# Kernel tuning notes

Hardware: AMD Instinct MI355X
Metric: run time of the kernel (lower is better)

The kernel has to match this reference:

```python
import jax, jax.numpy as jnp
import numpy as np

B, SQ, SE, H, NH = 2, 2048, 2048, 1024, 16
HD = H // NH  # 64

def setup_inputs() -> dict:
    key = jax.random.key(0)
    ks = jax.random.split(key, 8)
    s = 1.0 / np.sqrt(H)
    return {
        "hidden_states": jax.random.normal(ks[0], (B, SQ, H), jnp.float32),
        "encoder_hidden_states": jax.random.normal(ks[1], (B, SE, H), jnp.float32),
        "attention_mask": jnp.zeros((B, 1, 1, SQ + SE), jnp.float32),
        "Wq": jax.random.normal(ks[2], (H, H), jnp.float32) * s,
        "bq": jnp.zeros((H,), jnp.float32),
        "Wk": jax.random.normal(ks[3], (H, H), jnp.float32) * s,
        "bk": jnp.zeros((H,), jnp.float32),
        "Wv": jax.random.normal(ks[4], (H, H), jnp.float32) * s,
        "bv": jnp.zeros((H,), jnp.float32),
    }

def _split_heads(x):
    # [B, S, H] -> [B, NH, S, HD]
    b, s, _ = x.shape
    return x.reshape(b, s, NH, HD).transpose(0, 2, 1, 3)

def reference(hidden_states, encoder_hidden_states, attention_mask, Wq, bq, Wk, bk, Wv, bv):
    # Q from self tokens; K,V from concat(self, encoder) along sequence
    all_hs = jnp.concatenate([hidden_states, encoder_hidden_states], axis=1)  # [B, SQ+SE, H]
    q = _split_heads(hidden_states @ Wq + bq)   # [B, NH, SQ, HD]
    k = _split_heads(all_hs @ Wk + bk)          # [B, NH, SKV, HD]
    v = _split_heads(all_hs @ Wv + bv)          # [B, NH, SKV, HD]
    scores = jnp.einsum('bhqd,bhkd->bhqk', q, k) / jnp.sqrt(jnp.float32(HD))
    scores = scores + attention_mask            # additive mask, broadcast [B,1,1,SKV]
    probs = jax.nn.softmax(scores, axis=-1)     # dropout p=0 (eval)
    ctx = jnp.einsum('bhqk,bhkd->bhqd', probs, v)
    ctx = ctx.transpose(0, 2, 1, 3).reshape(hidden_states.shape[0], hidden_states.shape[1], H)
    return ctx
```

## Files before the change

### kernel.cpp

```cpp
#include <hip/hip_runtime.h>
#include <hip/hip_bf16.h>
#include <stdint.h>


typedef __attribute__((ext_vector_type(8))) short short8;
typedef __attribute__((ext_vector_type(4))) float f32x4;
typedef __attribute__((ext_vector_type(4))) unsigned short us4;

typedef __attribute__((ext_vector_type(8), may_alias)) short short8a;
typedef __attribute__((may_alias)) unsigned long long u64a;

#define MEMBAR() asm volatile("" ::: "memory")
#define DEV static __device__ __forceinline__

DEV unsigned short f2bf(float f) {
  unsigned int u = __builtin_bit_cast(unsigned int, f);
  u += 0x7fffu + ((u >> 16) & 1u);
  return (unsigned short)(u >> 16);
}

DEV float exp2_(float x) {
#if __has_builtin(__builtin_amdgcn_exp2f)
  return __builtin_amdgcn_exp2f(x);
#else
  float r; asm("v_exp_f32 %0, %1" : "=v"(r) : "v"(x)); return r;
#endif
}

DEV unsigned int cvtpk_bf16(float lo, float hi) {
  unsigned int r;
  asm("v_cvt_pk_bf16_f32 %0, %1, %2" : "=v"(r) : "v"(lo), "v"(hi));
  return r;
}

DEV void g2lds16(const void* g, void* l) {
  __builtin_amdgcn_global_load_lds((const __attribute__((address_space(1))) void*)g,
                                   (__attribute__((address_space(3))) void*)l, 16, 0, 0);
}

__global__ __launch_bounds__(256) void convert_allhs(const float* __restrict__ hid,
                                                     const float* __restrict__ enc,
                                                     unsigned short* __restrict__ ah) {
  int idx = blockIdx.x * 256 + threadIdx.x;
  const int perB = 4096 * 256;
  int b = idx / perB, r = idx - b * perB;
  int s = r >> 8, c4 = r & 255;
  const float* srcrow = (s < 2048) ? hid + (size_t)(b * 2048 + s) * 1024
                                   : enc + (size_t)(b * 2048 + (s - 2048)) * 1024;
  f32x4 v = *(const f32x4*)(srcrow + c4 * 4);
  us4 o;
  o[0] = f2bf(v[0]); o[1] = f2bf(v[1]); o[2] = f2bf(v[2]); o[3] = f2bf(v[3]);
  *(us4*)(ah + (size_t)idx * 4) = o;
}

__global__ __launch_bounds__(256) void premul_mask(const float* __restrict__ m,
                                                   float* __restrict__ o) {
  int i = blockIdx.x * 256 + threadIdx.x;
  o[i] = m[i] * 1.4426950408889634f;
}

__global__ __launch_bounds__(256) void transpose_w3(const float* __restrict__ Wq,
                                                    const float* __restrict__ Wk,
                                                    const float* __restrict__ Wv,
                                                    unsigned short* __restrict__ WtBase) {
  __shared__ unsigned short t[64][65];
  const int z = blockIdx.z;
  const float* W = (z == 0) ? Wq : (z == 1) ? Wk : Wv;
  unsigned short* Wt = WtBase + (size_t)z * 1048576;
  int k0 = blockIdx.y * 64, n0 = blockIdx.x * 64;
  int tid = threadIdx.x;
#pragma unroll
  for (int rep = 0; rep < 16; rep++) {
    int idx = rep * 256 + tid;
    int kk = idx >> 6, nn = idx & 63;
    t[kk][nn] = f2bf(W[(size_t)(k0 + kk) * 1024 + n0 + nn]);
  }
  __syncthreads();
#pragma unroll
  for (int rep = 0; rep < 16; rep++) {
    int idx = rep * 256 + tid;
    int nn = idx >> 6, kk = idx & 63;
    Wt[(size_t)(n0 + nn) * 1024 + k0 + kk] = t[kk][nn];
  }
}

__global__ __launch_bounds__(256) void gemm_all(const unsigned short* __restrict__ WTQ,
                                                const unsigned short* __restrict__ WTK,
                                                const unsigned short* __restrict__ WTV,
                                                const unsigned short* __restrict__ AH,
                                                const float* __restrict__ bq,
                                                const float* __restrict__ bk,
                                                const float* __restrict__ bv,
                                                unsigned short* __restrict__ Qout,
                                                unsigned short* __restrict__ Kout,
                                                unsigned short* __restrict__ Vout,
                                                float qscale) {
  __shared__ unsigned short ldsA[128 * 32];
  __shared__ unsigned short ldsB[128 * 32];

  int id = blockIdx.x;
  int f2 = (id & 7) * 160 + (id >> 3);

  const unsigned short *A, *Bm;
  const float* bias;
  unsigned short* outb;
  int S, mode, r0, c0;
  float osc = 1.0f;
  if (f2 < 256) {
    int t = f2;
    int b = t >> 7; t &= 127;
    c0 = (t & 15) * 128; r0 = (t >> 4) * 128;
    A = WTQ; Bm = AH + (size_t)b * 4194304; bias = bq;
    outb = Qout + (size_t)b * 2097152; S = 2048; mode = 0; osc = qscale;
  } else if (f2 < 768) {
    int t = f2 - 256;
    int b = t >> 8; t &= 255;
    c0 = (t & 31) * 128; r0 = (t >> 5) * 128;
    A = WTK; Bm = AH + (size_t)b * 4194304; bias = bk;
    outb = Kout + (size_t)b * 4194304; S = 4096; mode = 0;
  } else {
    int t = f2 - 768;
    int b = t >> 8; t &= 255;
    c0 = (t & 7) * 128; r0 = (t >> 3) * 128;
    A = AH + (size_t)b * 4194304; Bm = WTV; bias = bv;
    outb = Vout + (size_t)b * 4194304; S = 4096; mode = 1;
  }

  const int tid = threadIdx.x, w = tid >> 6, l = tid & 63;
  const int wr = w >> 1, wc = w & 1;
  const int lrow = l >> 2, lk = (l & 3) * 8;
  const int lc = l & 15, g = l >> 4;

  f32x4 acc[4][4];
#pragma unroll
  for (int i = 0; i < 4; i++)
#pragma unroll
    for (int j = 0; j < 4; j++) acc[i][j] = (f32x4){0.f, 0.f, 0.f, 0.f};

  for (int k0 = 0; k0 < 1024; k0 += 32) {
#pragma unroll
    for (int t = 0; t < 2; t++) {
      const int tt = w * 2 + t;
      g2lds16(A + (size_t)(r0 + tt * 16 + lrow) * 1024 + k0 + lk, (char*)ldsA + tt * 1024);
      g2lds16(Bm + (size_t)(c0 + tt * 16 + lrow) * 1024 + k0 + lk, (char*)ldsB + tt * 1024);
    }
    __syncthreads();
    short8 af[4], bf[4];
#pragma unroll
    for (int f = 0; f < 4; f++) {
      af[f] = *(const short8*)((const char*)ldsA + (wr * 64 + f * 16 + lc) * 64 + g * 16);
      bf[f] = *(const short8*)((const char*)ldsB + (wc * 64 + f * 16 + lc) * 64 + g * 16);
    }
#pragma unroll
    for (int fr = 0; fr < 4; fr++)
#pragma unroll
      for (int fc = 0; fc < 4; fc++)
        acc[fr][fc] = __builtin_amdgcn_mfma_f32_16x16x32_bf16(af[fr], bf[fc], acc[fr][fc], 0, 0, 0);
    __syncthreads();
  }

#pragma unroll
  for (int fr = 0; fr < 4; fr++) {
    int rb = r0 + wr * 64 + fr * 16 + g * 4;
    float bv4[4];
    if (mode == 0) {
#pragma unroll
      for (int i = 0; i < 4; i++) bv4[i] = bias[rb + i];
    }
#pragma unroll
    for (int fc = 0; fc < 4; fc++) {
      int c = c0 + wc * 64 + fc * 16 + lc;
      float bc = (mode == 0) ? 0.f : bias[c];
      us4 pk;
#pragma unroll
      for (int i = 0; i < 4; i++) {
        float v = (acc[fr][fc][i] + (mode == 0 ? bv4[i] : bc)) * osc;
        pk[i] = f2bf(v);
      }
      size_t addr;
      if (mode == 0) addr = ((size_t)(rb >> 6) * S + c) * 64 + (rb & 63);
      else           addr = (size_t)c * S + rb;
      *(us4*)(outb + addr) = pk;
    }
  }
}

__global__ __launch_bounds__(256) void attn_kernel(const unsigned short* __restrict__ Q,
                                                   const unsigned short* __restrict__ K,
                                                   const unsigned short* __restrict__ Vt,
                                                   const float* __restrict__ mask2,
                                                   float* __restrict__ out) {
  __shared__ __align__(16) char ldsKV[16384];
  __shared__ unsigned short plds[4096];
  char* ldsK = ldsKV;
  char* ldsV = ldsKV + 8192;

  int flat = blockIdx.x + 32 * (blockIdx.y + 16 * blockIdx.z);
  int xc = flat & 7, tt = flat >> 3;
  int f2 = xc * 64 + (tt & 63) + (tt >> 6) * 512;
  const int qt = f2 & 31, h = (f2 >> 5) & 15, b = f2 >> 9;

  const int tid = threadIdx.x, w = tid >> 6, l = tid & 63;
  const int lc = l & 15, g = l >> 4;

  const unsigned short* Qb = Q + ((size_t)(b * 16 + h) * 2048) * 64;
  const unsigned short* Kb = K + ((size_t)(b * 16 + h) * 4096) * 64;
  const unsigned short* Vb = Vt + ((size_t)(b * 16 + h) * 64) * 4096;
  const float* mk = mask2 + (size_t)b * 4096;
  const int sq0 = qt * 64 + w * 16;

  const int srow = l >> 3;
  const int schunk = (l & 7) ^ srow;

  short8 qf[2];
#pragma unroll
  for (int hh = 0; hh < 2; hh++)
    qf[hh] = *(const short8*)(Qb + (size_t)(sq0 + lc) * 64 + hh * 32 + g * 8);

  short8 ones;
#pragma unroll
  for (int i = 0; i < 8; i++) ones[i] = (short)0x3f80;

  f32x4 ctx[4];
#pragma unroll
  for (int df = 0; df < 4; df++) ctx[df] = (f32x4){0.f, 0.f, 0.f, 0.f};
  f32x4 lsacc = (f32x4){0.f, 0.f, 0.f, 0.f};

  char* pwave = (char*)plds + w * 2048;
  const int swz = (lc & 7) << 4;

  {
    short8 kreg[2], vreg[2];
#pragma unroll
    for (int c = 0; c < 2; c++) {
      int call = w * 2 + c;
      int r = call * 8 + srow;
      kreg[c] = *(const short8*)(Kb + (size_t)r * 64 + schunk * 8);
      vreg[c] = *(const short8*)(Vb + (size_t)r * 4096 + schunk * 8);
    }
#pragma unroll
    for (int c = 0; c < 2; c++) {
      int call = w * 2 + c;
      *(short8a*)(ldsK + call * 1024 + l * 16) = kreg[c];
      *(short8a*)(ldsV + call * 1024 + l * 16) = vreg[c];
    }
  }
  __syncthreads();

  for (int t = 0; t < 64; t++) {
    const int s0 = t * 64;

    f32x4 mvv[4];
#pragma unroll
    for (int f = 0; f < 4; f++)
      mvv[f] = *(const f32x4*)(mk + s0 + f * 16 + g * 4);

    short8 kreg[2], vreg[2];
    if (t < 63) {
#pragma unroll
      for (int c = 0; c < 2; c++) {
        int call = w * 2 + c;
        int r = call * 8 + srow;
        kreg[c] = *(const short8*)(Kb + (size_t)(s0 + 64 + r) * 64 + schunk * 8);
        vreg[c] = *(const short8*)(Vb + (size_t)r * 4096 + (s0 + 64) + schunk * 8);
      }
    }

#pragma unroll
    for (int f = 0; f < 4; f++) {
      short8 k0 = *(const short8*)(ldsK + (f * 16 + lc) * 128 + ((g ^ (lc & 7)) << 4));
      short8 k1 = *(const short8*)(ldsK + (f * 16 + lc) * 128 + (((4 + g) ^ (lc & 7)) << 4));
      f32x4 z = __builtin_amdgcn_mfma_f32_16x16x32_bf16(k0, qf[0], mvv[f], 0, 0, 0);
      z = __builtin_amdgcn_mfma_f32_16x16x32_bf16(k1, qf[1], z, 0, 0, 0);
      unsigned int lo = cvtpk_bf16(exp2_(z[0]), exp2_(z[1]));
      unsigned int hi = cvtpk_bf16(exp2_(z[2]), exp2_(z[3]));
      int base = lc * 128 + f * 32 + g * 8;
      *(u64a*)(pwave + (base ^ swz)) = ((unsigned long long)hi << 32) | lo;
    }

    MEMBAR();

    short8 pfrag[2];
#pragma unroll
    for (int kk = 0; kk < 2; kk++)
      pfrag[kk] = (short8)*(const short8a*)(pwave + ((lc * 128 + kk * 64 + g * 16) ^ swz));
#pragma unroll
    for (int df = 0; df < 4; df++) {
      short8 v0 = *(const short8*)(ldsV + (df * 16 + lc) * 128 + ((g ^ (lc & 7)) << 4));
      short8 v1 = *(const short8*)(ldsV + (df * 16 + lc) * 128 + (((4 + g) ^ (lc & 7)) << 4));
      ctx[df] = __builtin_amdgcn_mfma_f32_16x16x32_bf16(v0, pfrag[0], ctx[df], 0, 0, 0);
      ctx[df] = __builtin_amdgcn_mfma_f32_16x16x32_bf16(v1, pfrag[1], ctx[df], 0, 0, 0);
    }
    lsacc = __builtin_amdgcn_mfma_f32_16x16x32_bf16(ones, pfrag[0], lsacc, 0, 0, 0);
    lsacc = __builtin_amdgcn_mfma_f32_16x16x32_bf16(ones, pfrag[1], lsacc, 0, 0, 0);

    __syncthreads();

    if (t < 63) {
#pragma unroll
      for (int c = 0; c < 2; c++) {
        int call = w * 2 + c;
        *(short8a*)(ldsK + call * 1024 + l * 16) = kreg[c];
        *(short8a*)(ldsV + call * 1024 + l * 16) = vreg[c];
      }
      __syncthreads();
    }
  }

  float inv = 1.f / lsacc[0];
  size_t row = (size_t)(b * 2048 + sq0 + lc);
#pragma unroll
  for (int df = 0; df < 4; df++) {
    f32x4 o = ctx[df] * inv;
    *(f32x4*)(out + row * 1024 + h * 64 + df * 16 + g * 4) = o;
  }
}

extern "C" void kernel_launch(void* const* d_in, const int* in_sizes, int n_in,
                              void* d_out, int out_size, void* d_ws, size_t ws_size,
                              hipStream_t stream) {
  const float* hid = (const float*)d_in[0];
  const float* enc = (const float*)d_in[1];
  const float* mask = (const float*)d_in[2];
  const float* Wq = (const float*)d_in[3];
  const float* bq = (const float*)d_in[4];
  const float* Wk = (const float*)d_in[5];
  const float* bk = (const float*)d_in[6];
  const float* Wv = (const float*)d_in[7];
  const float* bv = (const float*)d_in[8];

  unsigned short* ws = (unsigned short*)d_ws;
  unsigned short* WTQ = ws;
  unsigned short* WTK = ws + 1048576;
  unsigned short* WTV = ws + 2097152;
  unsigned short* AH  = ws + 3145728;
  unsigned short* Qb  = ws + 11534336;
  unsigned short* Kb  = ws + 15728640;
  unsigned short* VT  = ws + 24117248;
  float* mask2 = (float*)(ws + 32505856);

  const float QSCALE = 0.18033688011112042f;

  convert_allhs<<<8192, 256, 0, stream>>>(hid, enc, AH);
  premul_mask<<<32, 256, 0, stream>>>(mask, mask2);
  transpose_w3<<<dim3(16, 16, 3), 256, 0, stream>>>(Wq, Wk, Wv, WTQ);

  gemm_all<<<1280, 256, 0, stream>>>(WTQ, WTK, WTV, AH, bq, bk, bv, Qb, Kb, VT, QSCALE);

  attn_kernel<<<dim3(32, 16, 2), 256, 0, stream>>>(Qb, Kb, VT, mask2, (float*)d_out);
}
```

Baseline: 196.7 us.

## Split KV sequence across wave pairs and give each wave two query tiles

The attention kernel now assigns each wave 32 query rows (two 16-row tiles) instead of 16, and splits the 4096-long KV range into two halves handled by different wave pairs. Each pair has its own K/V LDS buffers and runs 32 iterations instead of 64. Partial context and row sums are combined through LDS at the end. Because the exponent has no running max, the two halves add directly. The aim is to reuse each K/V fragment load across two query tiles and halve the serial loop length, at the cost of more registers, more LDS, and a final reduction step.

Result: slower. 201.2 us (+2.3%).

```diff
diff --git a/kernel.cpp b/kernel.cpp
--- a/kernel.cpp
+++ b/kernel.cpp
@@ -8,7 +8,9 @@
 typedef __attribute__((ext_vector_type(4))) unsigned short us4;
 
 typedef __attribute__((ext_vector_type(8), may_alias)) short short8a;
+typedef __attribute__((ext_vector_type(4), may_alias)) float f32x4a;
 typedef __attribute__((may_alias)) unsigned long long u64a;
+typedef __attribute__((may_alias)) float floata;
 
 #define MEMBAR() asm volatile("" ::: "memory")
 #define DEV static __device__ __forceinline__
@@ -190,10 +192,9 @@
                                                    const unsigned short* __restrict__ Vt,
                                                    const float* __restrict__ mask2,
                                                    float* __restrict__ out) {
-  __shared__ __align__(16) char ldsKV[16384];
-  __shared__ unsigned short plds[4096];
-  char* ldsK = ldsKV;
-  char* ldsV = ldsKV + 8192;
+  __shared__ __align__(16) char ldsK[2][8192];
+  __shared__ __align__(16) char ldsV[2][8192];
+  __shared__ __align__(16) char plds[16384];
 
   int flat = blockIdx.x + 32 * (blockIdx.y + 16 * blockIdx.z);
   int xc = flat & 7, tt = flat >> 3;
@@ -201,53 +202,60 @@
   const int qt = f2 & 31, h = (f2 >> 5) & 15, b = f2 >> 9;
 
   const int tid = threadIdx.x, w = tid >> 6, l = tid & 63;
+  const int rg = w & 1, kh = w >> 1;
   const int lc = l & 15, g = l >> 4;
 
   const unsigned short* Qb = Q + ((size_t)(b * 16 + h) * 2048) * 64;
-  const unsigned short* Kb = K + ((size_t)(b * 16 + h) * 4096) * 64;
-  const unsigned short* Vb = Vt + ((size_t)(b * 16 + h) * 64) * 4096;
-  const float* mk = mask2 + (size_t)b * 4096;
-  const int sq0 = qt * 64 + w * 16;
+  const unsigned short* Kb = K + ((size_t)((b * 16 + h) * 4096 + kh * 2048)) * 64;
+  const unsigned short* Vb = Vt + ((size_t)(b * 16 + h) * 64) * 4096 + kh * 2048;
+  const float* mk = mask2 + (size_t)b * 4096 + kh * 2048;
+  const int sq0 = qt * 64 + rg * 32;
 
   const int srow = l >> 3;
   const int schunk = (l & 7) ^ srow;
 
-  short8 qf[2];
-#pragma unroll
-  for (int hh = 0; hh < 2; hh++)
-    qf[hh] = *(const short8*)(Qb + (size_t)(sq0 + lc) * 64 + hh * 32 + g * 8);
+  short8 qf[2][2];
+#pragma unroll
+  for (int c2 = 0; c2 < 2; c2++)
+#pragma unroll
+    for (int hh = 0; hh < 2; hh++)
+      qf[c2][hh] = *(const short8*)(Qb + (size_t)(sq0 + c2 * 16 + lc) * 64 + hh * 32 + g * 8);
 
   short8 ones;
 #pragma unroll
   for (int i = 0; i < 8; i++) ones[i] = (short)0x3f80;
 
-  f32x4 ctx[4];
-#pragma unroll
-  for (int df = 0; df < 4; df++) ctx[df] = (f32x4){0.f, 0.f, 0.f, 0.f};
-  f32x4 lsacc = (f32x4){0.f, 0.f, 0.f, 0.f};
-
-  char* pwave = (char*)plds + w * 2048;
+  f32x4 ctx[2][4];
+#pragma unroll
+  for (int c2 = 0; c2 < 2; c2++)
+#pragma unroll
+    for (int df = 0; df < 4; df++) ctx[c2][df] = (f32x4){0.f, 0.f, 0.f, 0.f};
+  f32x4 lsacc[2];
+  lsacc[0] = (f32x4){0.f, 0.f, 0.f, 0.f};
+  lsacc[1] = (f32x4){0.f, 0.f, 0.f, 0.f};
+
+  char* kbase = ldsK[kh];
+  char* vbase = ldsV[kh];
+  char* pwave = plds + w * 4096;
   const int swz = (lc & 7) << 4;
 
   {
-    short8 kreg[2], vreg[2];
-#pragma unroll
-    for (int c = 0; c < 2; c++) {
-      int call = w * 2 + c;
-      int r = call * 8 + srow;
+    short8 kreg[4], vreg[4];
+#pragma unroll
+    for (int c = 0; c < 4; c++) {
+      int r = (rg * 4 + c) * 8 + srow;
       kreg[c] = *(const short8*)(Kb + (size_t)r * 64 + schunk * 8);
       vreg[c] = *(const short8*)(Vb + (size_t)r * 4096 + schunk * 8);
     }
 #pragma unroll
-    for (int c = 0; c < 2; c++) {
-      int call = w * 2 + c;
-      *(short8a*)(ldsK + call * 1024 + l * 16) = kreg[c];
-      *(short8a*)(ldsV + call * 1024 + l * 16) = vreg[c];
+    for (int c = 0; c < 4; c++) {
+      *(short8a*)(kbase + (rg * 4 + c) * 1024 + l * 16) = kreg[c];
+      *(short8a*)(vbase + (rg * 4 + c) * 1024 + l * 16) = vreg[c];
     }
   }
   __syncthreads();
 
-  for (int t = 0; t < 64; t++) {
+  for (int t = 0; t < 32; t++) {
     const int s0 = t * 64;
 
     f32x4 mvv[4];
@@ -255,12 +263,11 @@
     for (int f = 0; f < 4; f++)
       mvv[f] = *(const f32x4*)(mk + s0 + f * 16 + g * 4);
 
-    short8 kreg[2], vreg[2];
-    if (t < 63) {
-#pragma unroll
-      for (int c = 0; c < 2; c++) {
-        int call = w * 2 + c;
-        int r = call * 8 + srow;
+    short8 kreg[4], vreg[4];
+    if (t < 31) {
+#pragma unroll
+      for (int c = 0; c < 4; c++) {
+        int r = (rg * 4 + c) * 8 + srow;
         kreg[c] = *(const short8*)(Kb + (size_t)(s0 + 64 + r) * 64 + schunk * 8);
         vreg[c] = *(const short8*)(Vb + (size_t)r * 4096 + (s0 + 64) + schunk * 8);
       }
@@ -268,51 +275,84 @@
 
 #pragma unroll
     for (int f = 0; f < 4; f++) {
-      short8 k0 = *(const short8*)(ldsK + (f * 16 + lc) * 128 + ((g ^ (lc & 7)) << 4));
-      short8 k1 = *(const short8*)(ldsK + (f * 16 + lc) * 128 + (((4 + g) ^ (lc & 7)) << 4));
-      f32x4 z = __builtin_amdgcn_mfma_f32_16x16x32_bf16(k0, qf[0], mvv[f], 0, 0, 0);
-      z = __builtin_amdgcn_mfma_f32_16x16x32_bf16(k1, qf[1], z, 0, 0, 0);
-      unsigned int lo = cvtpk_bf16(exp2_(z[0]), exp2_(z[1]));
-      unsigned int hi = cvtpk_bf16(exp2_(z[2]), exp2_(z[3]));
-      int base = lc * 128 + f * 32 + g * 8;
-      *(u64a*)(pwave + (base ^ swz)) = ((unsigned long long)hi << 32) | lo;
+      short8 k0 = *(const short8*)(kbase + (f * 16 + lc) * 128 + ((g ^ (lc & 7)) << 4));
+      short8 k1 = *(const short8*)(kbase + (f * 16 + lc) * 128 + (((4 + g) ^ (lc & 7)) << 4));
+#pragma unroll
+      for (int c2 = 0; c2 < 2; c2++) {
+        f32x4 z = __builtin_amdgcn_mfma_f32_16x16x32_bf16(k0, qf[c2][0], mvv[f], 0, 0, 0);
+        z = __builtin_amdgcn_mfma_f32_16x16x32_bf16(k1, qf[c2][1], z, 0, 0, 0);
+        unsigned int lo = cvtpk_bf16(exp2_(z[0]), exp2_(z[1]));
+        unsigned int hi = cvtpk_bf16(exp2_(z[2]), exp2_(z[3]));
+        int base = lc * 128 + f * 32 + g * 8;
+        *(u64a*)(pwave + c2 * 2048 + (base ^ swz)) = ((unsigned long long)hi << 32) | lo;
+      }
     }
 
     MEMBAR();
 
-    short8 pfrag[2];
-#pragma unroll
-    for (int kk = 0; kk < 2; kk++)
-      pfrag[kk] = (short8)*(const short8a*)(pwave + ((lc * 128 + kk * 64 + g * 16) ^ swz));
+    short8 pfrag[2][2];
+#pragma unroll
+    for (int c2 = 0; c2 < 2; c2++)
+#pragma unroll
+      for (int kk = 0; kk < 2; kk++)
+        pfrag[c2][kk] = (short8)*(const short8a*)(pwave + c2 * 2048 + ((lc * 128 + kk * 64 + g * 16) ^ swz));
 #pragma unroll
     for (int df = 0; df < 4; df++) {
-      short8 v0 = *(const short8*)(ldsV + (df * 16 + lc) * 128 + ((g ^ (lc & 7)) << 4));
-      short8 v1 = *(const short8*)(ldsV + (df * 16 + lc) * 128 + (((4 + g) ^ (lc & 7)) << 4));
-      ctx[df] = __builtin_amdgcn_mfma_f32_16x16x32_bf16(v0, pfrag[0], ctx[df], 0, 0, 0);
-      ctx[df] = __builtin_amdgcn_mfma_f32_16x16x32_bf16(v1, pfrag[1], ctx[df], 0, 0, 0);
-    }
-    lsacc = __builtin_amdgcn_mfma_f32_16x16x32_bf16(ones, pfrag[0], lsacc, 0, 0, 0);
-    lsacc = __builtin_amdgcn_mfma_f32_16x16x32_bf16(ones, pfrag[1], lsacc, 0, 0, 0);
+      short8 v0 = *(const short8*)(vbase + (df * 16 + lc) * 128 + ((g ^ (lc & 7)) << 4));
+      short8 v1 = *(const short8*)(vbase + (df * 16 + lc) * 128 + (((4 + g) ^ (lc & 7)) << 4));
+#pragma unroll
+      for (int c2 = 0; c2 < 2; c2++) {
+        ctx[c2][df] = __builtin_amdgcn_mfma_f32_16x16x32_bf16(v0, pfrag[c2][0], ctx[c2][df], 0, 0, 0);
+        ctx[c2][df] = __builtin_amdgcn_mfma_f32_16x16x32_bf16(v1, pfrag[c2][1], ctx[c2][df], 0, 0, 0);
+      }
+    }
+#pragma unroll
+    for (int c2 = 0; c2 < 2; c2++) {
+      lsacc[c2] = __builtin_amdgcn_mfma_f32_16x16x32_bf16(ones, pfrag[c2][0], lsacc[c2], 0, 0, 0);
+      lsacc[c2] = __builtin_amdgcn_mfma_f32_16x16x32_bf16(ones, pfrag[c2][1], lsacc[c2], 0, 0, 0);
+    }
 
     __syncthreads();
 
-    if (t < 63) {
-#pragma unroll
-      for (int c = 0; c < 2; c++) {
-        int call = w * 2 + c;
-        *(short8a*)(ldsK + call * 1024 + l * 16) = kreg[c];
-        *(short8a*)(ldsV + call * 1024 + l * 16) = vreg[c];
+    if (t < 31) {
+#pragma unroll
+      for (int c = 0; c < 4; c++) {
+        *(short8a*)(kbase + (rg * 4 + c) * 1024 + l * 16) = kreg[c];
+        *(short8a*)(vbase + (rg * 4 + c) * 1024 + l * 16) = vreg[c];
       }
       __syncthreads();
     }
   }
 
-  float inv = 1.f / lsacc[0];
-  size_t row = (size_t)(b * 2048 + sq0 + lc);
-#pragma unroll
-  for (int df = 0; df < 4; df++) {
-    f32x4 o = ctx[df] * inv;
-    *(f32x4*)(out + row * 1024 + h * 64 + df * 16 + g * 4) = o;
+  float* mC = (float*)&ldsK[0][0];
+  float* lB = (float*)&plds[0];
+  if (kh == 1) {
+#pragma unroll
+    for (int c2 = 0; c2 < 2; c2++) {
+      int row = rg * 32 + c2 * 16 + lc;
+#pragma unroll
+      for (int df = 0; df < 4; df++) {
+        int slot = (df * 4 + g) ^ lc;
+        *(f32x4a*)(mC + row * 64 + slot * 4) = ctx[c2][df];
+      }
+      if (g == 0) *(floata*)(lB + row) = lsacc[c2][0];
+    }
+  }
+  __syncthreads();
+  if (kh == 0) {
+#pragma unroll
+    for (int c2 = 0; c2 < 2; c2++) {
+      int row = rg * 32 + c2 * 16 + lc;
+      float ls = lsacc[c2][0] + *(const floata*)(lB + row);
+      float inv = 1.f / ls;
+      size_t orow = (size_t)(b * 2048 + qt * 64 + row);
+#pragma unroll
+      for (int df = 0; df < 4; df++) {
+        int slot = (df * 4 + g) ^ lc;
+        f32x4 o = (ctx[c2][df] + *(const f32x4a*)(mC + row * 64 + slot * 4)) * inv;
+        *(f32x4*)(out + orow * 1024 + h * 64 + df * 16 + g * 4) = o;
+      }
+    }
   }
 }
 
```
